# Optimization experiments

Measured on AMD Instinct MI355X. Metric: run time of the kernel, lower is better.

The kernel has to match this reference:

```python
import jax, jax.numpy as jnp
import numpy as np

B, S, D, H, DFF = 2, 2048, 1024, 16, 4096
HD = D // H
EPS = 1e-5


def setup_inputs() -> dict:
    key = jax.random.key(0)
    ks = jax.random.split(key, 8)
    s = lambda fan_in: 1.0 / np.sqrt(fan_in)
    return {
        "x": jax.random.normal(ks[0], (B, S, D), jnp.float32),
        "ln1_g": jnp.ones((D,), jnp.float32),
        "ln1_b": jnp.zeros((D,), jnp.float32),
        "Wq": jax.random.normal(ks[1], (D, D), jnp.float32) * s(D),
        "Wk": jax.random.normal(ks[2], (D, D), jnp.float32) * s(D),
        "Wv": jax.random.normal(ks[3], (D, D), jnp.float32) * s(D),
        "Wo": jax.random.normal(ks[4], (D, D), jnp.float32) * s(D),
        "bo": jnp.zeros((D,), jnp.float32),
        "ln2_g": jnp.ones((D,), jnp.float32),
        "ln2_b": jnp.zeros((D,), jnp.float32),
        "W1": jax.random.normal(ks[5], (D, DFF), jnp.float32) * s(D),
        "b1": jnp.zeros((DFF,), jnp.float32),
        "W2": jax.random.normal(ks[6], (DFF, D), jnp.float32) * s(DFF),
        "b2": jnp.zeros((D,), jnp.float32),
    }


def _layernorm(x, g, b):
    mu = jnp.mean(x, axis=-1, keepdims=True)
    var = jnp.var(x, axis=-1, keepdims=True)
    return (x - mu) * jax.lax.rsqrt(var + EPS) * g + b


def reference(x, ln1_g, ln1_b, Wq, Wk, Wv, Wo, bo, ln2_g, ln2_b, W1, b1, W2, b2):
    # --- pre-LN + causal multi-head attention + residual ---
    h = _layernorm(x, ln1_g, ln1_b)
    q = (h @ Wq).reshape(B, S, H, HD).transpose(0, 2, 1, 3)  # [B,H,S,hd]
    k = (h @ Wk).reshape(B, S, H, HD).transpose(0, 2, 1, 3)
    v = (h @ Wv).reshape(B, S, H, HD).transpose(0, 2, 1, 3)
    scores = jnp.einsum("bhqd,bhkd->bhqk", q, k) / jnp.sqrt(jnp.float32(HD))
    causal = jnp.triu(jnp.ones((S, S), bool), k=1)  # True above diagonal -> masked
    scores = jnp.where(causal, -jnp.inf, scores)
    attn = jax.nn.softmax(scores, axis=-1)  # dropout is identity at inference
    ctx = jnp.einsum("bhqk,bhkd->bhqd", attn, v)
    ctx = ctx.transpose(0, 2, 1, 3).reshape(B, S, D)
    x = x + ctx @ Wo + bo
    # --- pre-LN + MLP + residual ---
    h = _layernorm(x, ln2_g, ln2_b)
    h = jax.nn.gelu(h @ W1 + b1, approximate=False)  # torch nn.GELU default = exact
    x = x + h @ W2 + b2
    return x
```

## Files before the change

### kernel.cpp

```cpp
#include <hip/hip_runtime.h>
#include <hip/hip_bf16.h>
#include <math.h>

using bf16 = __hip_bfloat16;
typedef short bf16x8 __attribute__((ext_vector_type(8)));
typedef float f32x4 __attribute__((ext_vector_type(4)));

static constexpr int B = 2, S = 2048, D = 1024, H = 16, HD = 64, DFF = 4096;
static constexpr int NR = B * S;
static constexpr int DQ = 3072;
static constexpr float EPS = 1e-5f;

__device__ __forceinline__ bf16 f2b(float v) { return __float2bfloat16(v); }

typedef __attribute__((address_space(1))) const void* gp1_t;
typedef __attribute__((address_space(3))) void* sp3_t;
__device__ __forceinline__ void gld_lds16(const bf16* g, bf16* l) {
    __builtin_amdgcn_global_load_lds((gp1_t)(const void*)g, (sp3_t)(void*)l, 16, 0, 0);
}

__global__ __launch_bounds__(256) void convT_kernel(const float* __restrict__ src,
                                                    bf16* __restrict__ dst,
                                                    int K, int N) {
    __shared__ float tile[64][65];
    const int k0 = blockIdx.x * 64, n0 = blockIdx.y * 64;
    const int tid = threadIdx.x;
    const int r = tid >> 4, c = (tid & 15) * 4;
#pragma unroll
    for (int rr = 0; rr < 64; rr += 16) {
        float4 v = *(const float4*)&src[(size_t)(k0 + r + rr) * N + n0 + c];
        tile[r + rr][c] = v.x; tile[r + rr][c + 1] = v.y;
        tile[r + rr][c + 2] = v.z; tile[r + rr][c + 3] = v.w;
    }
    __syncthreads();
    const int n = tid >> 2, ks = (tid & 3) * 16;
    union { bf16 h[16]; int4 v2[2]; } o;
#pragma unroll
    for (int i = 0; i < 16; ++i) o.h[i] = f2b(tile[ks + i][n]);
    bf16* dp = &dst[(size_t)(n0 + n) * K + k0 + ks];
    *(int4*)dp = o.v2[0];
    *(int4*)(dp + 8) = o.v2[1];
}

__global__ __launch_bounds__(256) void ln_kernel(const float* __restrict__ x,
                                                 const float* __restrict__ g,
                                                 const float* __restrict__ b,
                                                 bf16* __restrict__ out) {
    const int row = blockIdx.x;
    const int tid = threadIdx.x;
    const float4 v4 = ((const float4*)(x + (size_t)row * D))[tid];
    float v[4] = {v4.x, v4.y, v4.z, v4.w};
    float s = v[0] + v[1] + v[2] + v[3];
    float sq = v[0] * v[0] + v[1] * v[1] + v[2] * v[2] + v[3] * v[3];
#pragma unroll
    for (int off = 32; off >= 1; off >>= 1) {
        s += __shfl_xor(s, off);
        sq += __shfl_xor(sq, off);
    }
    __shared__ float ssum[4], ssq[4];
    const int wave = tid >> 6;
    if ((tid & 63) == 0) { ssum[wave] = s; ssq[wave] = sq; }
    __syncthreads();
    s = ssum[0] + ssum[1] + ssum[2] + ssum[3];
    sq = ssq[0] + ssq[1] + ssq[2] + ssq[3];
    const float mu = s * (1.0f / D);
    const float var = sq * (1.0f / D) - mu * mu;
    const float rstd = rsqrtf(var + EPS);
    bf16* orow = out + (size_t)row * D;
#pragma unroll
    for (int i = 0; i < 4; ++i) {
        const int c = tid * 4 + i;
        orow[c] = f2b((v[i] - mu) * rstd * g[c] + b[c]);
    }
}

template <int EPI>
__global__ __launch_bounds__(512) void gemm256(const bf16* __restrict__ A,
                                               const bf16* __restrict__ Bt,
                                               const float* __restrict__ bias,
                                               bf16* __restrict__ C,
                                               int M, int N, int K) {
    constexpr int ASZ = 256 * 32, BSZ = 128 * 32;
    constexpr int CST = 128 + 8;
    __shared__ __align__(16) bf16 smem[2 * (ASZ + BSZ)];

    const int Mtiles = M / 256;
    const int p = blockIdx.x;
    const int tm = p % Mtiles;
    const int tn = p / Mtiles;
    const int tid = threadIdx.x;
    const int wave = tid >> 6, lane = tid & 63;
    const int wm = wave >> 1, wn = wave & 1;
    const int quad = lane >> 4, l16 = lane & 15;

    f32x4 acc[4][4];
#pragma unroll
    for (int i = 0; i < 4; ++i)
#pragma unroll
        for (int j = 0; j < 4; ++j) acc[i][j] = (f32x4){0.f, 0.f, 0.f, 0.f};

    const int s_row = tid >> 2, s_seg = (tid & 3) * 8;
    const bf16* ApLo = A + (size_t)(tm * 256 + s_row) * K + s_seg;
    const size_t K128 = (size_t)128 * K;
    const bf16* Bp = Bt + (size_t)(tn * 128 + s_row) * K + s_seg;

    gld_lds16(ApLo, smem + tid * 8);
    gld_lds16(ApLo + K128, smem + (512 + tid) * 8);
    gld_lds16(Bp, smem + 2 * ASZ + tid * 8);
    ApLo += 32;
    Bp += 32;

    const int nk = K / 32;
    for (int kt = 0; kt < nk; ++kt) {
        const int cur = kt & 1, nxt = cur ^ 1;
        bf16* Acur = smem + cur * ASZ;
        bf16* Bcur = smem + 2 * ASZ + cur * BSZ;
        __syncthreads();
        if (kt + 1 < nk) {
            bf16* Anxt = smem + nxt * ASZ;
            bf16* Bnxt = smem + 2 * ASZ + nxt * BSZ;
            gld_lds16(ApLo, Anxt + tid * 8);
            gld_lds16(ApLo + K128, Anxt + (512 + tid) * 8);
            gld_lds16(Bp, Bnxt + tid * 8);
            ApLo += 32;
            Bp += 32;
        }

        bf16x8 aF[4], bF[4];
#pragma unroll
        for (int mt = 0; mt < 4; ++mt)
            aF[mt] = *(const bf16x8*)(Acur + (wm * 64 + mt * 16 + l16) * 32 + quad * 8);
#pragma unroll
        for (int nt = 0; nt < 4; ++nt)
            bF[nt] = *(const bf16x8*)(Bcur + (wn * 64 + nt * 16 + l16) * 32 + quad * 8);
#pragma unroll
        for (int mt = 0; mt < 4; ++mt)
#pragma unroll
            for (int nt = 0; nt < 4; ++nt)
                acc[mt][nt] = __builtin_amdgcn_mfma_f32_16x16x32_bf16(
                    aF[mt], bF[nt], acc[mt][nt], 0, 0, 0);
    }

#pragma unroll
    for (int hh = 0; hh < 2; ++hh) {
        __syncthreads();
        if ((wm >> 1) == hh) {
#pragma unroll
            for (int nt = 0; nt < 4; ++nt) {
                const int ccol = wn * 64 + nt * 16 + l16;
                float bv = 0.f;
                if (EPI == 2) bv = bias[tn * 128 + ccol];
#pragma unroll
                for (int mt = 0; mt < 4; ++mt) {
                    const int r0 = (wm & 1) * 64 + mt * 16 + quad * 4;
#pragma unroll
                    for (int j = 0; j < 4; ++j) {
                        float v = acc[mt][nt][j];
                        if (EPI == 2) {
                            v += bv;
                            v = 0.5f * v * (1.0f + erff(v * 0.70710678118654752f));
                        }
                        smem[(r0 + j) * CST + ccol] = f2b(v);
                    }
                }
            }
        }
        __syncthreads();
        bf16* crow = C + (size_t)(tm * 256 + hh * 128) * N + tn * 128;
#pragma unroll
        for (int i = 0; i < 4; ++i) {
            const int gid = i * 512 + tid;
            const int row = gid >> 4, c8 = gid & 15;
            const int4 val = *(const int4*)(smem + row * CST + c8 * 8);
            *(int4*)(crow + (size_t)row * N + c8 * 8) = val;
        }
    }
}

template <int EPI, int BN, int TPB>
__global__ __launch_bounds__(256) void gemm_bt(const bf16* __restrict__ A,
                                               const bf16* __restrict__ Bt,
                                               const float* __restrict__ bias,
                                               const float* __restrict__ res,
                                               void* __restrict__ Cv,
                                               int M, int N, int K) {
    constexpr int NTW = BN / 32;
    constexpr int ASZ = 128 * 32, BSZ = BN * 32;
    __shared__ __align__(16) bf16 smem[2 * (ASZ + BSZ)];

    const int Mtiles = M / 128;
    const int p = blockIdx.x;
    const int tm = p % Mtiles;
    const int tn0 = (p / Mtiles) * TPB;
    const int tid = threadIdx.x;
    const int wave = tid >> 6, lane = tid & 63;
    const int wm = wave >> 1, wn = wave & 1;
    const int quad = lane >> 4, l16 = lane & 15;

    const int s_row = tid >> 2, s_seg = (tid & 3) * 8;
    const size_t K64 = (size_t)64 * K;
    const int nk = K / 32;

    for (int tp = 0; tp < TPB; ++tp) {
        const int tn = tn0 + tp;
        if (tp) __syncthreads();

        f32x4 acc[4][NTW];
#pragma unroll
        for (int i = 0; i < 4; ++i)
#pragma unroll
            for (int j = 0; j < NTW; ++j) acc[i][j] = (f32x4){0.f, 0.f, 0.f, 0.f};

        const bf16* Ap = A + (size_t)(tm * 128 + s_row) * K + s_seg;
        const bf16* Bp = Bt + (size_t)(tn * BN + s_row) * K + s_seg;

        gld_lds16(Ap, smem + tid * 8);
        gld_lds16(Ap + K64, smem + (256 + tid) * 8);
        gld_lds16(Bp, smem + 2 * ASZ + tid * 8);
        if constexpr (BN == 128) gld_lds16(Bp + K64, smem + 2 * ASZ + (256 + tid) * 8);
        Ap += 32;
        Bp += 32;

        for (int kt = 0; kt < nk; ++kt) {
            const int cur = kt & 1, nxt = cur ^ 1;
            bf16* Acur = smem + cur * ASZ;
            bf16* Bcur = smem + 2 * ASZ + cur * BSZ;
            __syncthreads();
            if (kt + 1 < nk) {
                bf16* Anxt = smem + nxt * ASZ;
                bf16* Bnxt = smem + 2 * ASZ + nxt * BSZ;
                gld_lds16(Ap, Anxt + tid * 8);
                gld_lds16(Ap + K64, Anxt + (256 + tid) * 8);
                gld_lds16(Bp, Bnxt + tid * 8);
                if constexpr (BN == 128) gld_lds16(Bp + K64, Bnxt + (256 + tid) * 8);
                Ap += 32;
                Bp += 32;
            }

            bf16x8 aF[4], bF[NTW];
#pragma unroll
            for (int mt = 0; mt < 4; ++mt)
                aF[mt] = *(const bf16x8*)(Acur + (wm * 64 + mt * 16 + l16) * 32 + quad * 8);
#pragma unroll
            for (int nt = 0; nt < NTW; ++nt)
                bF[nt] = *(const bf16x8*)(Bcur + (wn * (BN / 2) + nt * 16 + l16) * 32 + quad * 8);
#pragma unroll
            for (int mt = 0; mt < 4; ++mt)
#pragma unroll
                for (int nt = 0; nt < NTW; ++nt)
                    acc[mt][nt] = __builtin_amdgcn_mfma_f32_16x16x32_bf16(
                        aF[mt], bF[nt], acc[mt][nt], 0, 0, 0);
        }

#pragma unroll
        for (int nt = 0; nt < NTW; ++nt) {
            const int col = tn * BN + wn * (BN / 2) + nt * 16 + l16;
            const float bv = bias[col];
#pragma unroll
            for (int mt = 0; mt < 4; ++mt) {
                const int row0 = tm * 128 + wm * 64 + mt * 16 + quad * 4;
#pragma unroll
                for (int j = 0; j < 4; ++j) {
                    const size_t idx = (size_t)(row0 + j) * N + col;
                    ((float*)Cv)[idx] = acc[mt][nt][j] + bv + res[idx];
                }
            }
        }
    }
}

__global__ __launch_bounds__(512) void fattn_kernel(const bf16* __restrict__ QKV,
                                                    bf16* __restrict__ ctx) {
    const int id = blockIdx.x;
    const int bh = id & 31;
    const int k = id >> 5;
    const int t = (k < 8) ? 15 - k : k - 8;
    const int b = bh >> 4, h = bh & (H - 1);
    const int tid = threadIdx.x;
    const int wave = tid >> 6, lane = tid & 63;
    const int quad = lane >> 4, l16 = lane & 15;
    const bf16* Qp = QKV + (size_t)b * S * DQ + h * HD;
    const bf16* Kp = Qp + D;
    const bf16* Vp = Qp + 2 * D;

    __shared__ __align__(16) bf16 Ks[2][64 * 64];
    __shared__ __align__(16) bf16 Vt[2][64][72];
    __shared__ __align__(16) bf16 Ps[128][76];

    const int keyA = tid >> 3, dsA = ((tid & 7) ^ (keyA & 7)) * 8;

    const int q0 = t * 128;
    const bf16* qg = Qp + (size_t)(q0 + wave * 16 + l16) * DQ + quad * 8;
    union U8 { bf16 h[8]; bf16x8 v; };
    U8 uq0, uq1;
    uq0.v = *(const bf16x8*)(qg);
    uq1.v = *(const bf16x8*)(qg + 32);
#pragma unroll
    for (int i = 0; i < 8; ++i) {
        uq0.h[i] = f2b(__bfloat162float(uq0.h[i]) * 0.125f);
        uq1.h[i] = f2b(__bfloat162float(uq1.h[i]) * 0.125f);
    }
    const bf16x8 aQ0 = uq0.v;
    const bf16x8 aQ1 = uq1.v;

    f32x4 O[4];
#pragma unroll
    for (int nt = 0; nt < 4; ++nt) O[nt] = (f32x4){0.f, 0.f, 0.f, 0.f};
    float rowm = -3.0e38f, rowl = 0.f;

    gld_lds16(Kp + (size_t)keyA * DQ + dsA, Ks[0] + tid * 8);
    {
        const bf16* vg = Vp + (size_t)lane * DQ + wave * 8;
        union { int4 v; bf16 hh[8]; } u;
        u.v = *(const int4*)vg;
#pragma unroll
        for (int i = 0; i < 8; ++i) Vt[0][wave * 8 + i][lane] = u.hh[i];
    }

    const int nch = 2 * t + 2;
    for (int c = 0; c < nch; ++c) {
        const int cur = c & 1, nxt = cur ^ 1;
        __syncthreads();
        union { int4 v; bf16 hh[8]; } u;
        if (c < nch - 1) {
            const int k1 = (c + 1) * 64;
            gld_lds16(Kp + (size_t)(k1 + keyA) * DQ + dsA, Ks[nxt] + tid * 8);
            u.v = *(const int4*)(Vp + (size_t)(k1 + lane) * DQ + wave * 8);
        }

        f32x4 sc[4];
#pragma unroll
        for (int nt = 0; nt < 4; ++nt) {
            const int r = nt * 16 + l16;
            const bf16x8 bK0 = *(const bf16x8*)(Ks[cur] + (r * 8 + (quad ^ (r & 7))) * 8);
            const bf16x8 bK1 = *(const bf16x8*)(Ks[cur] + (r * 8 + ((4 + quad) ^ (r & 7))) * 8);
            f32x4 z = (f32x4){0.f, 0.f, 0.f, 0.f};
            z = __builtin_amdgcn_mfma_f32_16x16x32_bf16(bK0, aQ0, z, 0, 0, 0);
            z = __builtin_amdgcn_mfma_f32_16x16x32_bf16(bK1, aQ1, z, 0, 0, 0);
            sc[nt] = z;
        }
        if (c >= 2 * t) {
            const int kb0 = (c - 2 * t) * 64 + quad * 4;
            const int qr = wave * 16 + l16;
#pragma unroll
            for (int nt = 0; nt < 4; ++nt)
#pragma unroll
                for (int j = 0; j < 4; ++j)
                    if (kb0 + nt * 16 + j > qr) sc[nt][j] = -3.0e38f;
        }
        f32x4 mv;
#pragma unroll
        for (int j = 0; j < 4; ++j)
            mv[j] = fmaxf(fmaxf(sc[0][j], sc[1][j]), fmaxf(sc[2][j], sc[3][j]));
        float mx = fmaxf(fmaxf(mv[0], mv[1]), fmaxf(mv[2], mv[3]));
        mx = fmaxf(mx, __shfl_xor(mx, 16));
        mx = fmaxf(mx, __shfl_xor(mx, 32));
        const float mn = fmaxf(rowm, mx);
        const float alq = __expf(rowm - mn);
        rowm = mn;
        float rs = 0.f;
#pragma unroll
        for (int nt = 0; nt < 4; ++nt)
#pragma unroll
            for (int j = 0; j < 4; ++j) {
                sc[nt][j] = __expf(sc[nt][j] - mn);
                rs += sc[nt][j];
            }
        rs += __shfl_xor(rs, 16);
        rs += __shfl_xor(rs, 32);
        rowl = rowl * alq + rs;

        const int prow = wave * 16 + l16;
#pragma unroll
        for (int nt = 0; nt < 4; ++nt) {
            union { bf16 h[4]; int2 v; } pk;
#pragma unroll
            for (int j = 0; j < 4; ++j) pk.h[j] = f2b(sc[nt][j]);
            *(int2*)&Ps[prow][nt * 16 + quad * 4] = pk.v;
        }
        asm volatile("s_waitcnt lgkmcnt(0)" ::: "memory");
        const bf16x8 aP0 = *(const bf16x8*)&Ps[prow][quad * 8];
        const bf16x8 aP1 = *(const bf16x8*)&Ps[prow][32 + quad * 8];
#pragma unroll
        for (int nt = 0; nt < 4; ++nt)
#pragma unroll
            for (int j = 0; j < 4; ++j) O[nt][j] *= alq;
#pragma unroll
        for (int nt = 0; nt < 4; ++nt) {
            const bf16x8 bV0 = *(const bf16x8*)&Vt[cur][nt * 16 + l16][quad * 8];
            const bf16x8 bV1 = *(const bf16x8*)&Vt[cur][nt * 16 + l16][32 + quad * 8];
            O[nt] = __builtin_amdgcn_mfma_f32_16x16x32_bf16(bV0, aP0, O[nt], 0, 0, 0);
            O[nt] = __builtin_amdgcn_mfma_f32_16x16x32_bf16(bV1, aP1, O[nt], 0, 0, 0);
        }
        if (c < nch - 1) {
#pragma unroll
            for (int i = 0; i < 8; ++i) Vt[nxt][wave * 8 + i][lane] = u.hh[i];
        }
    }

    const float rlq = 1.0f / rowl;
    bf16* crow = ctx + (size_t)b * S * D + h * HD + (size_t)(q0 + wave * 16 + l16) * D;
#pragma unroll
    for (int nt = 0; nt < 4; ++nt) {
        union { bf16 h[4]; int2 v; } o;
#pragma unroll
        for (int j = 0; j < 4; ++j) o.h[j] = f2b(O[nt][j] * rlq);
        *(int2*)(crow + nt * 16 + quad * 4) = o.v;
    }
}

extern "C" void kernel_launch(void* const* d_in, const int* in_sizes, int n_in,
                              void* d_out, int out_size, void* d_ws, size_t ws_size,
                              hipStream_t stream) {
    const float* x     = (const float*)d_in[0];
    const float* ln1_g = (const float*)d_in[1];
    const float* ln1_b = (const float*)d_in[2];
    const float* Wq    = (const float*)d_in[3];
    const float* Wk    = (const float*)d_in[4];
    const float* Wv    = (const float*)d_in[5];
    const float* Wo    = (const float*)d_in[6];
    const float* bo    = (const float*)d_in[7];
    const float* ln2_g = (const float*)d_in[8];
    const float* ln2_b = (const float*)d_in[9];
    const float* W1    = (const float*)d_in[10];
    const float* b1    = (const float*)d_in[11];
    const float* W2    = (const float*)d_in[12];
    const float* b2    = (const float*)d_in[13];
    float* out = (float*)d_out;

    char* ws = (char*)d_ws;
    const size_t MB = (size_t)1 << 20;
    bf16* h     = (bf16*)(ws + 0 * MB);
    bf16* W1T   = (bf16*)(ws + 0 * MB);
    bf16* QKVb  = (bf16*)(ws + 8 * MB);
    bf16* hff   = (bf16*)(ws + 8 * MB);
    bf16* ctx   = (bf16*)(ws + 32 * MB);
    bf16* h2    = (bf16*)(ws + 40 * MB);
    bf16* WqkvT = (bf16*)(ws + 48 * MB);
    bf16* WoT   = (bf16*)(ws + 54 * MB);
    bf16* W2T   = (bf16*)(ws + 56 * MB);

    dim3 gt(16, 16);
    convT_kernel<<<gt, 256, 0, stream>>>(Wq, WqkvT,                 D, D);
    convT_kernel<<<gt, 256, 0, stream>>>(Wk, WqkvT + (size_t)D * D, D, D);
    convT_kernel<<<gt, 256, 0, stream>>>(Wv, WqkvT + (size_t)2 * D * D, D, D);
    convT_kernel<<<gt, 256, 0, stream>>>(Wo, WoT, D, D);
    convT_kernel<<<dim3(64, 16), 256, 0, stream>>>(W2, W2T, DFF, D);
    ln_kernel<<<NR, 256, 0, stream>>>(x, ln1_g, ln1_b, h);
    gemm256<0><<<(NR / 256) * (DQ / 128), 512, 0, stream>>>(
        h, WqkvT, nullptr, QKVb, NR, DQ, D);
    convT_kernel<<<dim3(16, 64), 256, 0, stream>>>(W1, W1T, D, DFF);
    fattn_kernel<<<dim3((S / 128) * B * H), 512, 0, stream>>>(QKVb, ctx);
    gemm_bt<1, 64, 1><<<(NR / 128) * (D / 64), 256, 0, stream>>>(
        ctx, WoT, bo, x, out, NR, D, D);
    ln_kernel<<<NR, 256, 0, stream>>>(out, ln2_g, ln2_b, h2);
    gemm256<2><<<(NR / 256) * (DFF / 128), 512, 0, stream>>>(
        h2, W1T, b1, hff, NR, DFF, D);
    gemm_bt<1, 64, 1><<<(NR / 128) * (D / 64), 256, 0, stream>>>(
        hff, W2T, b2, out, out, NR, D, DFF);
}
```

Baseline: 360.2 us.

## Split-K the W2 down-projection GEMM with a separate reduction kernel

The final MLP GEMM (K=4096) is split into two K halves using 128-wide N tiles, each writing fp32 partials to workspace. A new reduce kernel then sums the partials with bias and residual. This changes the tile count and gives more blocks per unit of K work, so the long-K GEMM has shorter per-block loops and better occupancy. The cost is 32MB of extra partial-sum traffic and one more kernel launch. It falls back to the old path if the workspace is too small.

```diff
diff --git a/kernel.cpp b/kernel.cpp
--- a/kernel.cpp
+++ b/kernel.cpp
@@ -183,13 +183,16 @@
                                                const float* __restrict__ bias,
                                                const float* __restrict__ res,
                                                void* __restrict__ Cv,
-                                               int M, int N, int K) {
+                                               int M, int N, int K, int Kld) {
     constexpr int NTW = BN / 32;
     constexpr int ASZ = 128 * 32, BSZ = BN * 32;
     __shared__ __align__(16) bf16 smem[2 * (ASZ + BSZ)];
 
     const int Mtiles = M / 128;
-    const int p = blockIdx.x;
+    const int T = Mtiles * (N / BN) / TPB;
+    const int p0 = blockIdx.x;
+    const int ks = p0 / T;
+    const int p = p0 % T;
     const int tm = p % Mtiles;
     const int tn0 = (p / Mtiles) * TPB;
     const int tid = threadIdx.x;
@@ -197,8 +200,11 @@
     const int wm = wave >> 1, wn = wave & 1;
     const int quad = lane >> 4, l16 = lane & 15;
 
+    A += (size_t)ks * K;
+    Bt += (size_t)ks * K;
+
     const int s_row = tid >> 2, s_seg = (tid & 3) * 8;
-    const size_t K64 = (size_t)64 * K;
+    const size_t K64 = (size_t)64 * Kld;
     const int nk = K / 32;
 
     for (int tp = 0; tp < TPB; ++tp) {
@@ -211,8 +217,8 @@
 #pragma unroll
             for (int j = 0; j < NTW; ++j) acc[i][j] = (f32x4){0.f, 0.f, 0.f, 0.f};
 
-        const bf16* Ap = A + (size_t)(tm * 128 + s_row) * K + s_seg;
-        const bf16* Bp = Bt + (size_t)(tn * BN + s_row) * K + s_seg;
+        const bf16* Ap = A + (size_t)(tm * 128 + s_row) * Kld + s_seg;
+        const bf16* Bp = Bt + (size_t)(tn * BN + s_row) * Kld + s_seg;
 
         gld_lds16(Ap, smem + tid * 8);
         gld_lds16(Ap + K64, smem + (256 + tid) * 8);
@@ -252,21 +258,54 @@
                         aF[mt], bF[nt], acc[mt][nt], 0, 0, 0);
         }
 
-#pragma unroll
-        for (int nt = 0; nt < NTW; ++nt) {
-            const int col = tn * BN + wn * (BN / 2) + nt * 16 + l16;
-            const float bv = bias[col];
-#pragma unroll
-            for (int mt = 0; mt < 4; ++mt) {
-                const int row0 = tm * 128 + wm * 64 + mt * 16 + quad * 4;
-#pragma unroll
-                for (int j = 0; j < 4; ++j) {
-                    const size_t idx = (size_t)(row0 + j) * N + col;
-                    ((float*)Cv)[idx] = acc[mt][nt][j] + bv + res[idx];
+        if constexpr (EPI == 1) {
+#pragma unroll
+            for (int nt = 0; nt < NTW; ++nt) {
+                const int col = tn * BN + wn * (BN / 2) + nt * 16 + l16;
+                const float bv = bias[col];
+#pragma unroll
+                for (int mt = 0; mt < 4; ++mt) {
+                    const int row0 = tm * 128 + wm * 64 + mt * 16 + quad * 4;
+#pragma unroll
+                    for (int j = 0; j < 4; ++j) {
+                        const size_t idx = (size_t)(row0 + j) * N + col;
+                        ((float*)Cv)[idx] = acc[mt][nt][j] + bv + res[idx];
+                    }
                 }
             }
-        }
-    }
+        } else {
+            float* P = (float*)Cv + (size_t)ks * M * N;
+#pragma unroll
+            for (int nt = 0; nt < NTW; ++nt) {
+                const int col = tn * BN + wn * (BN / 2) + nt * 16 + l16;
+#pragma unroll
+                for (int mt = 0; mt < 4; ++mt) {
+                    const int row0 = tm * 128 + wm * 64 + mt * 16 + quad * 4;
+#pragma unroll
+                    for (int j = 0; j < 4; ++j)
+                        P[(size_t)(row0 + j) * N + col] = acc[mt][nt][j];
+                }
+            }
+        }
+    }
+}
+
+__global__ __launch_bounds__(256) void reduce2_kernel(float* __restrict__ out,
+                                                      const float* __restrict__ p0,
+                                                      const float* __restrict__ p1,
+                                                      const float* __restrict__ bias,
+                                                      const float* __restrict__ res) {
+    const size_t i4 = ((size_t)blockIdx.x * 256 + threadIdx.x) * 4;
+    const float4 a = *(const float4*)(p0 + i4);
+    const float4 b = *(const float4*)(p1 + i4);
+    const float4 r = *(const float4*)(res + i4);
+    const float4 bv = *(const float4*)(bias + ((int)i4 & (D - 1)));
+    float4 o;
+    o.x = a.x + b.x + r.x + bv.x;
+    o.y = a.y + b.y + r.y + bv.y;
+    o.z = a.z + b.z + r.z + bv.z;
+    o.w = a.w + b.w + r.w + bv.w;
+    *(float4*)(out + i4) = o;
 }
 
 __global__ __launch_bounds__(512) void fattn_kernel(const bf16* __restrict__ QKV,
@@ -439,6 +478,7 @@
     bf16* WqkvT = (bf16*)(ws + 48 * MB);
     bf16* WoT   = (bf16*)(ws + 54 * MB);
     bf16* W2T   = (bf16*)(ws + 56 * MB);
+    float* pK   = (float*)(ws + 64 * MB);
 
     dim3 gt(16, 16);
     convT_kernel<<<gt, 256, 0, stream>>>(Wq, WqkvT,                 D, D);
@@ -452,10 +492,17 @@
     convT_kernel<<<dim3(16, 64), 256, 0, stream>>>(W1, W1T, D, DFF);
     fattn_kernel<<<dim3((S / 128) * B * H), 512, 0, stream>>>(QKVb, ctx);
     gemm_bt<1, 64, 1><<<(NR / 128) * (D / 64), 256, 0, stream>>>(
-        ctx, WoT, bo, x, out, NR, D, D);
+        ctx, WoT, bo, x, out, NR, D, D, D);
     ln_kernel<<<NR, 256, 0, stream>>>(out, ln2_g, ln2_b, h2);
     gemm256<2><<<(NR / 256) * (DFF / 128), 512, 0, stream>>>(
         h2, W1T, b1, hff, NR, DFF, D);
-    gemm_bt<1, 64, 1><<<(NR / 128) * (D / 64), 256, 0, stream>>>(
-        hff, W2T, b2, out, out, NR, D, DFF);
-}
+    if (ws_size >= 96 * MB) {
+        gemm_bt<3, 128, 1><<<(NR / 128) * (D / 128) * 2, 256, 0, stream>>>(
+            hff, W2T, nullptr, nullptr, pK, NR, D, DFF / 2, DFF);
+        reduce2_kernel<<<NR * D / 1024, 256, 0, stream>>>(
+            out, pK, pK + (size_t)NR * D, b2, out);
+    } else {
+        gemm_bt<1, 64, 1><<<(NR / 128) * (D / 64), 256, 0, stream>>>(
+            hff, W2T, b2, out, out, NR, D, DFF, DFF);
+    }
+}
```

After: 366.5 us. About the same (+1.7%).

## Shrink attention query tile, keep P in registers, merge weight transposes

Applied to the files above, without the earlier changes.

The attention kernel moves from 128-query blocks of 8 waves to 64-query blocks of 4 waves. Key rows are permuted within each tile so the MFMA score output already matches the operand layout of the PV MFMA. That lets P stay in registers instead of taking a round trip through shared memory, and s_setprio is raised around the MFMA sections. The five separate weight transpose launches are also merged into one kernel to cut launch overhead. The trade-off is twice as many attention blocks, each doing less work per K/V tile load, which lowers reuse of the loaded tiles.

```diff
diff --git a/kernel.cpp b/kernel.cpp
--- a/kernel.cpp
+++ b/kernel.cpp
@@ -19,12 +19,10 @@
     __builtin_amdgcn_global_load_lds((gp1_t)(const void*)g, (sp3_t)(void*)l, 16, 0, 0);
 }
 
-__global__ __launch_bounds__(256) void convT_kernel(const float* __restrict__ src,
-                                                    bf16* __restrict__ dst,
-                                                    int K, int N) {
+__device__ __forceinline__ void convT_body(const float* __restrict__ src,
+                                           bf16* __restrict__ dst,
+                                           int K, int N, int k0, int n0, int tid) {
     __shared__ float tile[64][65];
-    const int k0 = blockIdx.x * 64, n0 = blockIdx.y * 64;
-    const int tid = threadIdx.x;
     const int r = tid >> 4, c = (tid & 15) * 4;
 #pragma unroll
     for (int rr = 0; rr < 64; rr += 16) {
@@ -40,6 +38,39 @@
     bf16* dp = &dst[(size_t)(n0 + n) * K + k0 + ks];
     *(int4*)dp = o.v2[0];
     *(int4*)(dp + 8) = o.v2[1];
+}
+
+__global__ __launch_bounds__(256) void convT_kernel(const float* __restrict__ src,
+                                                    bf16* __restrict__ dst,
+                                                    int K, int N) {
+    convT_body(src, dst, K, N, blockIdx.x * 64, blockIdx.y * 64, threadIdx.x);
+}
+
+__global__ __launch_bounds__(256) void convT5_kernel(const float* __restrict__ Wq,
+                                                     const float* __restrict__ Wk,
+                                                     const float* __restrict__ Wv,
+                                                     const float* __restrict__ Wo,
+                                                     const float* __restrict__ W2,
+                                                     bf16* __restrict__ WqkvT,
+                                                     bf16* __restrict__ WoT,
+                                                     bf16* __restrict__ W2T) {
+    const int bid = blockIdx.x;
+    const float* src;
+    bf16* dst;
+    int K, N, bx, by;
+    if (bid < 768) {
+        const int j = bid >> 8, r = bid & 255;
+        src = (j == 0) ? Wq : ((j == 1) ? Wk : Wv);
+        dst = WqkvT + (size_t)j * D * D;
+        K = D; N = D; bx = r & 15; by = r >> 4;
+    } else if (bid < 1024) {
+        const int r = bid - 768;
+        src = Wo; dst = WoT; K = D; N = D; bx = r & 15; by = r >> 4;
+    } else {
+        const int r = bid - 1024;
+        src = W2; dst = W2T; K = DFF; N = D; bx = r & 63; by = r >> 6;
+    }
+    convT_body(src, dst, K, N, bx * 64, by * 64, threadIdx.x);
 }
 
 __global__ __launch_bounds__(256) void ln_kernel(const float* __restrict__ x,
@@ -269,12 +300,12 @@
     }
 }
 
-__global__ __launch_bounds__(512) void fattn_kernel(const bf16* __restrict__ QKV,
+__global__ __launch_bounds__(256) void fattn_kernel(const bf16* __restrict__ QKV,
                                                     bf16* __restrict__ ctx) {
     const int id = blockIdx.x;
     const int bh = id & 31;
     const int k = id >> 5;
-    const int t = (k < 8) ? 15 - k : k - 8;
+    const int t = (k < 16) ? 31 - k : k - 16;
     const int b = bh >> 4, h = bh & (H - 1);
     const int tid = threadIdx.x;
     const int wave = tid >> 6, lane = tid & 63;
@@ -285,11 +316,13 @@
 
     __shared__ __align__(16) bf16 Ks[2][64 * 64];
     __shared__ __align__(16) bf16 Vt[2][64][72];
-    __shared__ __align__(16) bf16 Ps[128][76];
-
-    const int keyA = tid >> 3, dsA = ((tid & 7) ^ (keyA & 7)) * 8;
-
-    const int q0 = t * 128;
+
+    const int keyA = tid >> 3;
+    const int sA = (keyA & 3) | ((keyA >> 1) & 4);
+    const int dsA = ((tid & 7) ^ sA) * 8;
+    const size_t K32 = (size_t)32 * DQ;
+
+    const int q0 = t * 64;
     const bf16* qg = Qp + (size_t)(q0 + wave * 16 + l16) * DQ + quad * 8;
     union U8 { bf16 h[8]; bf16x8 v; };
     U8 uq0, uq1;
@@ -303,50 +336,66 @@
     const bf16x8 aQ0 = uq0.v;
     const bf16x8 aQ1 = uq1.v;
 
+    const int kb = (l16 >> 2) * 8 + (l16 & 3);
+    const int sQ = (l16 & 3) | (((l16 >> 2) & 1) << 2);
+    const int ofs0 = kb * 64 + ((quad ^ sQ) * 8);
+    const int ofs1 = kb * 64 + (((4 + quad) ^ sQ) * 8);
+
     f32x4 O[4];
 #pragma unroll
     for (int nt = 0; nt < 4; ++nt) O[nt] = (f32x4){0.f, 0.f, 0.f, 0.f};
     float rowm = -3.0e38f, rowl = 0.f;
 
     gld_lds16(Kp + (size_t)keyA * DQ + dsA, Ks[0] + tid * 8);
+    gld_lds16(Kp + K32 + (size_t)keyA * DQ + dsA, Ks[0] + (256 + tid) * 8);
     {
-        const bf16* vg = Vp + (size_t)lane * DQ + wave * 8;
-        union { int4 v; bf16 hh[8]; } u;
-        u.v = *(const int4*)vg;
-#pragma unroll
-        for (int i = 0; i < 8; ++i) Vt[0][wave * 8 + i][lane] = u.hh[i];
-    }
-
-    const int nch = 2 * t + 2;
+        const bf16* vg = Vp + (size_t)lane * DQ + wave * 16;
+        U8 u0, u1;
+        u0.v = *(const bf16x8*)vg;
+        u1.v = *(const bf16x8*)(vg + 8);
+#pragma unroll
+        for (int i = 0; i < 8; ++i) {
+            Vt[0][wave * 16 + i][lane] = u0.h[i];
+            Vt[0][wave * 16 + 8 + i][lane] = u1.h[i];
+        }
+    }
+
+    const int nch = t + 1;
     for (int c = 0; c < nch; ++c) {
         const int cur = c & 1, nxt = cur ^ 1;
         __syncthreads();
-        union { int4 v; bf16 hh[8]; } u;
-        if (c < nch - 1) {
-            const int k1 = (c + 1) * 64;
-            gld_lds16(Kp + (size_t)(k1 + keyA) * DQ + dsA, Ks[nxt] + tid * 8);
-            u.v = *(const int4*)(Vp + (size_t)(k1 + lane) * DQ + wave * 8);
+        U8 u0, u1;
+        if (c + 1 < nch) {
+            const bf16* kg = Kp + (size_t)((c + 1) * 64 + keyA) * DQ + dsA;
+            gld_lds16(kg, Ks[nxt] + tid * 8);
+            gld_lds16(kg + K32, Ks[nxt] + (256 + tid) * 8);
+            const bf16* vg = Vp + (size_t)((c + 1) * 64 + lane) * DQ + wave * 16;
+            u0.v = *(const bf16x8*)vg;
+            u1.v = *(const bf16x8*)(vg + 8);
         }
 
         f32x4 sc[4];
-#pragma unroll
-        for (int nt = 0; nt < 4; ++nt) {
-            const int r = nt * 16 + l16;
-            const bf16x8 bK0 = *(const bf16x8*)(Ks[cur] + (r * 8 + (quad ^ (r & 7))) * 8);
-            const bf16x8 bK1 = *(const bf16x8*)(Ks[cur] + (r * 8 + ((4 + quad) ^ (r & 7))) * 8);
+        __builtin_amdgcn_s_setprio(1);
+#pragma unroll
+        for (int m = 0; m < 4; ++m) {
+            const bf16* kr = Ks[cur] + (m & 1) * 256 + (m >> 1) * 2048;
+            const bf16x8 bK0 = *(const bf16x8*)(kr + ofs0);
+            const bf16x8 bK1 = *(const bf16x8*)(kr + ofs1);
             f32x4 z = (f32x4){0.f, 0.f, 0.f, 0.f};
             z = __builtin_amdgcn_mfma_f32_16x16x32_bf16(bK0, aQ0, z, 0, 0, 0);
             z = __builtin_amdgcn_mfma_f32_16x16x32_bf16(bK1, aQ1, z, 0, 0, 0);
-            sc[nt] = z;
-        }
-        if (c >= 2 * t) {
-            const int kb0 = (c - 2 * t) * 64 + quad * 4;
-            const int qr = wave * 16 + l16;
-#pragma unroll
-            for (int nt = 0; nt < 4; ++nt)
+            sc[m] = z;
+        }
+        __builtin_amdgcn_s_setprio(0);
+        if (c == nch - 1) {
+            const int qloc = wave * 16 + l16;
+#pragma unroll
+            for (int m = 0; m < 4; ++m) {
+                const int kk = quad * 8 + (m & 1) * 4 + (m >> 1) * 32;
 #pragma unroll
                 for (int j = 0; j < 4; ++j)
-                    if (kb0 + nt * 16 + j > qr) sc[nt][j] = -3.0e38f;
+                    if (kk + j > qloc) sc[m][j] = -3.0e38f;
+            }
         }
         f32x4 mv;
 #pragma unroll
@@ -360,41 +409,43 @@
         rowm = mn;
         float rs = 0.f;
 #pragma unroll
-        for (int nt = 0; nt < 4; ++nt)
+        for (int m = 0; m < 4; ++m)
 #pragma unroll
             for (int j = 0; j < 4; ++j) {
-                sc[nt][j] = __expf(sc[nt][j] - mn);
-                rs += sc[nt][j];
+                sc[m][j] = __expf(sc[m][j] - mn);
+                rs += sc[m][j];
             }
         rs += __shfl_xor(rs, 16);
         rs += __shfl_xor(rs, 32);
         rowl = rowl * alq + rs;
 
-        const int prow = wave * 16 + l16;
-#pragma unroll
-        for (int nt = 0; nt < 4; ++nt) {
-            union { bf16 h[4]; int2 v; } pk;
-#pragma unroll
-            for (int j = 0; j < 4; ++j) pk.h[j] = f2b(sc[nt][j]);
-            *(int2*)&Ps[prow][nt * 16 + quad * 4] = pk.v;
-        }
-        asm volatile("s_waitcnt lgkmcnt(0)" ::: "memory");
-        const bf16x8 aP0 = *(const bf16x8*)&Ps[prow][quad * 8];
-        const bf16x8 aP1 = *(const bf16x8*)&Ps[prow][32 + quad * 8];
+        U8 p0, p1;
+#pragma unroll
+        for (int j = 0; j < 4; ++j) {
+            p0.h[j]     = f2b(sc[0][j]);
+            p0.h[4 + j] = f2b(sc[1][j]);
+            p1.h[j]     = f2b(sc[2][j]);
+            p1.h[4 + j] = f2b(sc[3][j]);
+        }
 #pragma unroll
         for (int nt = 0; nt < 4; ++nt)
 #pragma unroll
             for (int j = 0; j < 4; ++j) O[nt][j] *= alq;
+        __builtin_amdgcn_s_setprio(1);
 #pragma unroll
         for (int nt = 0; nt < 4; ++nt) {
             const bf16x8 bV0 = *(const bf16x8*)&Vt[cur][nt * 16 + l16][quad * 8];
             const bf16x8 bV1 = *(const bf16x8*)&Vt[cur][nt * 16 + l16][32 + quad * 8];
-            O[nt] = __builtin_amdgcn_mfma_f32_16x16x32_bf16(bV0, aP0, O[nt], 0, 0, 0);
-            O[nt] = __builtin_amdgcn_mfma_f32_16x16x32_bf16(bV1, aP1, O[nt], 0, 0, 0);
-        }
-        if (c < nch - 1) {
-#pragma unroll
-            for (int i = 0; i < 8; ++i) Vt[nxt][wave * 8 + i][lane] = u.hh[i];
+            O[nt] = __builtin_amdgcn_mfma_f32_16x16x32_bf16(bV0, p0.v, O[nt], 0, 0, 0);
+            O[nt] = __builtin_amdgcn_mfma_f32_16x16x32_bf16(bV1, p1.v, O[nt], 0, 0, 0);
+        }
+        __builtin_amdgcn_s_setprio(0);
+        if (c + 1 < nch) {
+#pragma unroll
+            for (int i = 0; i < 8; ++i) {
+                Vt[nxt][wave * 16 + i][lane] = u0.h[i];
+                Vt[nxt][wave * 16 + 8 + i][lane] = u1.h[i];
+            }
         }
     }
 
@@ -440,17 +491,12 @@
     bf16* WoT   = (bf16*)(ws + 54 * MB);
     bf16* W2T   = (bf16*)(ws + 56 * MB);
 
-    dim3 gt(16, 16);
-    convT_kernel<<<gt, 256, 0, stream>>>(Wq, WqkvT,                 D, D);
-    convT_kernel<<<gt, 256, 0, stream>>>(Wk, WqkvT + (size_t)D * D, D, D);
-    convT_kernel<<<gt, 256, 0, stream>>>(Wv, WqkvT + (size_t)2 * D * D, D, D);
-    convT_kernel<<<gt, 256, 0, stream>>>(Wo, WoT, D, D);
-    convT_kernel<<<dim3(64, 16), 256, 0, stream>>>(W2, W2T, DFF, D);
+    convT5_kernel<<<2048, 256, 0, stream>>>(Wq, Wk, Wv, Wo, W2, WqkvT, WoT, W2T);
     ln_kernel<<<NR, 256, 0, stream>>>(x, ln1_g, ln1_b, h);
     gemm256<0><<<(NR / 256) * (DQ / 128), 512, 0, stream>>>(
         h, WqkvT, nullptr, QKVb, NR, DQ, D);
     convT_kernel<<<dim3(16, 64), 256, 0, stream>>>(W1, W1T, D, DFF);
-    fattn_kernel<<<dim3((S / 128) * B * H), 512, 0, stream>>>(QKVb, ctx);
+    fattn_kernel<<<dim3((S / 64) * B * H), 256, 0, stream>>>(QKVb, ctx);
     gemm_bt<1, 64, 1><<<(NR / 128) * (D / 64), 256, 0, stream>>>(
         ctx, WoT, bo, x, out, NR, D, D);
     ln_kernel<<<NR, 256, 0, stream>>>(out, ln2_g, ln2_b, h2);
```

After: 355.5 us. About the same (-1.3%).
